# Optimization experiments

Hardware: AMD Instinct MI355X
Metric: run time of the kernel (lower is better)

The kernel has to match this reference:

```python
import jax, jax.numpy as jnp
import numpy as np

ORDER = 128


def setup_inputs() -> dict:
    key = jax.random.key(0)
    k1, k2 = jax.random.split(key)
    B, T, p, Tf = 16, 131072, ORDER, 8192
    excitation = jax.random.normal(k1, (B, T), dtype=jnp.float32)
    # reflection coefficients in (-1, 1)
    rc = jax.random.uniform(k2, (B, p, Tf), dtype=jnp.float32, minval=-1.0, maxval=1.0)
    return {"excitation": excitation, "rc": rc}


def _rc_to_lpc(rc):
    """Step-up (Levinson-Durbin) recursion: reflection coeffs -> LPC coeffs.

    rc: (B, p, T_f)  ->  a: (B, T_f, p+1) with a[..., 0] == 1.
    Each step i does a[..., 1:i+2] += k_i * flip(a[..., :i+1]).
    Implemented as a full-width masked gather so it runs in one lax.scan.
    """
    B, p, Tf = rc.shape
    ks = jnp.transpose(rc, (1, 0, 2))  # (p, B, Tf)
    a0 = jnp.zeros((B, Tf, p + 1), rc.dtype).at[..., 0].set(1.0)
    j = jnp.arange(p + 1)

    def step(a, inp):
        i, k = inp  # i: scalar order index, k: (B, Tf)
        src = jnp.clip(i + 1 - j, 0, p)
        a_rev = jnp.take(a, src, axis=-1)          # flipped prefix, full width
        mask = (j >= 1) & (j <= i + 1)             # only positions 1..i+1 update
        a = a + jnp.where(mask, k[..., None] * a_rev, jnp.zeros((), a.dtype))
        return a, None

    a, _ = jax.lax.scan(step, a0, (jnp.arange(p), ks))
    return a


def reference(excitation, rc):
    # forward: rc = rc * 0.98, then step-up recursion to LPC coefficients.
    # (the original module's FFT synthesis path is dead code and the audio
    #  passthrough is the identity; the live math is the recursion below)
    rc = rc * 0.98
    return _rc_to_lpc(rc)
```

## Files before the change

### kernel.cpp

```cpp
#include <hip/hip_runtime.h>


#define NB    16
#define ORD   128
#define TF    8192

__global__ __launch_bounds__(256, 2)
void lpc_stepup_kernel(const float* __restrict__ rc, float* __restrict__ out) {
    const int tid = threadIdx.x;
    const int gid = blockIdx.x * 256 + tid;
    const int b = gid >> 13;
    const int t = gid & (TF - 1);

    const float* rcp = rc + ((size_t)b * ORD) * TF + t;

    float a[ORD + 1];
    a[0] = 1.0f;

#pragma unroll
    for (int m = 1; m <= ORD; ++m) {
        const float k = 0.98f * rcp[(size_t)(m - 1) * TF];
#pragma unroll
        for (int j = 1; 2 * j < m; ++j) {
            const float lo = a[j];
            const float hi = a[m - j];
            a[j]     = fmaf(k, hi, lo);
            a[m - j] = fmaf(k, lo, hi);
        }
        if ((m & 1) == 0) {
            const float mid = a[m >> 1];
            a[m >> 1] = fmaf(k, mid, mid);
        }
        a[m] = k;
    }

    __shared__ __align__(16) float lds[64 * (ORD + 1)];
    const int my_round = tid >> 6;
    const int row      = tid & 63;
    float* out_block = out + (size_t)blockIdx.x * 256 * (ORD + 1);

    for (int r = 0; r < 4; ++r) {
        __syncthreads();
        if (my_round == r) {
#pragma unroll
            for (int j = 0; j <= ORD; ++j)
                lds[row * (ORD + 1) + j] = a[j];
        }
        __syncthreads();
        const float4* lds4 = (const float4*)lds;
        float4* out4 = (float4*)(out_block + (size_t)r * 64 * (ORD + 1));
        for (int e = tid; e < (64 * (ORD + 1)) / 4; e += 256)
            out4[e] = lds4[e];
    }
}

extern "C" void kernel_launch(void* const* d_in, const int* in_sizes, int n_in,
                              void* d_out, int out_size, void* d_ws, size_t ws_size,
                              hipStream_t stream) {
    const float* rc = (const float*)d_in[1];
    float* out = (float*)d_out;
    dim3 grid((NB * TF) / 256);
    dim3 block(256);
    hipLaunchKernelGGL(lpc_stepup_kernel, grid, block, 0, stream, rc, out);
}
```

Baseline: 140.8 us.

## Prefetch reflection coefficients and use single-wave blocks with chunked LDS output

Reflection coefficients are now loaded through a 16-deep register ring that prefetches ahead, so global-load latency is hidden behind the recursion arithmetic. Blocks shrink to a single 64-thread wave, which removes the four-round serialized LDS staging across waves. The output is staged through a padded 64x33 LDS tile in 32-column chunks to avoid bank conflicts, with the final column written directly. In exchange the output stores become scalar instead of float4 and the coefficient ring adds register pressure.

```diff
diff --git a/kernel.cpp b/kernel.cpp
--- a/kernel.cpp
+++ b/kernel.cpp
@@ -1,25 +1,31 @@
 #include <hip/hip_runtime.h>
 
 
-#define NB    16
-#define ORD   128
-#define TF    8192
+#define NB   16
+#define ORD  128
+#define TF   8192
+#define PD   16
 
-__global__ __launch_bounds__(256, 2)
+__global__ __launch_bounds__(64, 1)
 void lpc_stepup_kernel(const float* __restrict__ rc, float* __restrict__ out) {
     const int tid = threadIdx.x;
-    const int gid = blockIdx.x * 256 + tid;
+    const int gid = blockIdx.x * 64 + tid;
     const int b = gid >> 13;
     const int t = gid & (TF - 1);
+    const float* rcp = rc + ((size_t)b * ORD) * TF + t;
 
-    const float* rcp = rc + ((size_t)b * ORD) * TF + t;
+    float kq[PD];
+#pragma unroll
+    for (int i = 0; i < PD; ++i) kq[i] = rcp[(size_t)i * TF];
 
     float a[ORD + 1];
     a[0] = 1.0f;
 
 #pragma unroll
     for (int m = 1; m <= ORD; ++m) {
-        const float k = 0.98f * rcp[(size_t)(m - 1) * TF];
+        const float k = 0.98f * kq[(m - 1) & (PD - 1)];
+        if (m - 1 + PD < ORD)
+            kq[(m - 1) & (PD - 1)] = rcp[(size_t)(m - 1 + PD) * TF];
 #pragma unroll
         for (int j = 1; 2 * j < m; ++j) {
             const float lo = a[j];
@@ -34,24 +40,22 @@
         a[m] = k;
     }
 
-    __shared__ __align__(16) float lds[64 * (ORD + 1)];
-    const int my_round = tid >> 6;
-    const int row      = tid & 63;
-    float* out_block = out + (size_t)blockIdx.x * 256 * (ORD + 1);
+    __shared__ float lds[64 * 33];
+    float* outb = out + (size_t)blockIdx.x * 64 * (ORD + 1);
 
-    for (int r = 0; r < 4; ++r) {
+#pragma unroll
+    for (int c = 0; c < 4; ++c) {
         __syncthreads();
-        if (my_round == r) {
 #pragma unroll
-            for (int j = 0; j <= ORD; ++j)
-                lds[row * (ORD + 1) + j] = a[j];
+        for (int j = 0; j < 32; ++j)
+            lds[tid * 33 + j] = a[c * 32 + j];
+        __syncthreads();
+        for (int e = tid; e < 2048; e += 64) {
+            const int r = e >> 5, q = e & 31;
+            outb[r * (ORD + 1) + c * 32 + q] = lds[r * 33 + q];
         }
-        __syncthreads();
-        const float4* lds4 = (const float4*)lds;
-        float4* out4 = (float4*)(out_block + (size_t)r * 64 * (ORD + 1));
-        for (int e = tid; e < (64 * (ORD + 1)) / 4; e += 256)
-            out4[e] = lds4[e];
     }
+    outb[tid * (ORD + 1) + ORD] = a[ORD];
 }
 
 extern "C" void kernel_launch(void* const* d_in, const int* in_sizes, int n_in,
@@ -59,7 +63,7 @@
                               hipStream_t stream) {
     const float* rc = (const float*)d_in[1];
     float* out = (float*)d_out;
-    dim3 grid((NB * TF) / 256);
-    dim3 block(256);
+    dim3 grid((NB * TF) / 64);
+    dim3 block(64);
     hipLaunchKernelGGL(lpc_stepup_kernel, grid, block, 0, stream, rc, out);
 }
```

After: 144.7 us. +2.8%, slower.
